# Performance work log

Hardware: AMD Instinct MI355X
Metric: run time of the kernel (lower is better)

## Reference

```python
import jax, jax.numpy as jnp
import numpy as np

N_NODES = 50000
N_EDGES = 600000
D = 128
R = 8
EPS = 1e-5


def layer_norm(x, g, b):
    mu = jnp.mean(x, axis=-1, keepdims=True)
    var = jnp.mean(jnp.square(x - mu), axis=-1, keepdims=True)
    return (x - mu) * jax.lax.rsqrt(var + EPS) * g + b


def rgcn(x, src, dst, edge_attr, W, root, bias, num_nodes):
    # x: [N, d], W: [R, d, f], edge_attr: [E, R] soft relation weights
    E = src.shape[0]
    f = W.shape[-1]
    msg = jnp.zeros((E, f), dtype=x.dtype)
    for r in range(W.shape[0]):  # small fixed relation count
        hr = x @ W[r]                       # [N, f]
        msg = msg + hr[src] * edge_attr[:, r][:, None]  # gather + weight
    agg = jax.ops.segment_sum(msg, dst, num_segments=num_nodes)  # scatter-add
    return agg + x @ root + bias


def setup_inputs() -> dict:
    key = jax.random.key(0)
    ks = jax.random.split(key, 12)
    s = 1.0 / np.sqrt(D)
    return {
        "x": jax.random.normal(ks[0], (N_NODES, D), dtype=jnp.float32),
        "edge_index": jax.random.randint(ks[1], (2, N_EDGES), 0, N_NODES, dtype=jnp.int64),
        "edge_attr": jax.random.uniform(ks[2], (N_EDGES, R), dtype=jnp.float32),
        "ln1_g": jnp.ones((D,), jnp.float32),
        "ln1_b": jnp.zeros((D,), jnp.float32),
        "W1": jax.random.normal(ks[3], (R, D, D), jnp.float32) * s,
        "root1": jax.random.normal(ks[4], (D, D), jnp.float32) * s,
        "b1": jnp.zeros((D,), jnp.float32),
        "ln2_g": jnp.ones((D,), jnp.float32),
        "ln2_b": jnp.zeros((D,), jnp.float32),
        "W2": jax.random.normal(ks[5], (R, D, D), jnp.float32) * s,
        "root2": jax.random.normal(ks[6], (D, D), jnp.float32) * s,
        "b2": jnp.zeros((D,), jnp.float32),
    }


def reference(x, edge_index, edge_attr, ln1_g, ln1_b, W1, root1, b1,
              ln2_g, ln2_b, W2, root2, b2):
    src, dst = edge_index[0], edge_index[1]
    identity = x
    out = jax.nn.gelu(layer_norm(x, ln1_g, ln1_b), approximate=False)
    out = rgcn(out, src, dst, edge_attr, W1, root1, b1, x.shape[0])
    out = jax.nn.gelu(layer_norm(out, ln2_g, ln2_b), approximate=False)
    out = rgcn(out, src, dst, edge_attr, W2, root2, b2, x.shape[0])
    return out + identity
```

## Files before the change

### kernel.cpp

```cpp
#include <hip/hip_runtime.h>
#include <hip/hip_bf16.h>

typedef __attribute__((ext_vector_type(8))) short short8;
typedef __attribute__((ext_vector_type(4))) float f32x4;

#define LDA 1152

__device__ __forceinline__ float bf2f(unsigned short u) {
    union { unsigned int i; float f; } v; v.i = ((unsigned int)u) << 16; return v.f;
}
__device__ __forceinline__ unsigned short f2bf(float f) {
    __hip_bfloat16 h = __float2bfloat16(f);
    union { __hip_bfloat16 h; unsigned short u; } v; v.h = h; return v.u;
}
__device__ __forceinline__ float gelu_exact(float t) {
    return 0.5f * t * (1.0f + erff(t * 0.70710678118654752f));
}

__global__ void prep_all(const float* __restrict__ W1, const float* __restrict__ root1,
                         unsigned short* __restrict__ Bf1,
                         const float* __restrict__ W2, const float* __restrict__ root2,
                         unsigned short* __restrict__ Bf2,
                         int* __restrict__ cnt, int cntB,
                         const float* __restrict__ x, const float* __restrict__ g,
                         const float* __restrict__ bvec, unsigned short* __restrict__ A,
                         int N) {
    int b = blockIdx.x;
    if (b < 1152) {
        int i = b * 256 + threadIdx.x;
        const float* W = W1; const float* root = root1; unsigned short* Bfrag = Bf1;
        if (i >= 1152 * 128) { i -= 1152 * 128; W = W2; root = root2; Bfrag = Bf2; }
        int kp = i >> 7, n = i & 127;
        float v;
        if (kp < 1024) {
            int d = kp >> 3, r = kp & 7;
            v = W[((size_t)r * 128 + d) * 128 + n];
        } else {
            v = root[(size_t)(kp - 1024) * 128 + n];
        }
        int kb = kp >> 5;
        int lane = (((kp >> 3) & 3) << 4) | (n & 15);
        int j = kp & 7;
        int t = n >> 4;
        Bfrag[(((size_t)(kb * 8 + t) * 64 + lane) << 3) + j] = f2bf(v);
        return;
    }
    if (b < 1152 + cntB) {
        int zi = (b - 1152) * 256 + threadIdx.x;
        cnt[zi] = 0;
        return;
    }
    int row = (((b - 1152 - cntB) * 256) + threadIdx.x) >> 6;
    if (row >= N) return;
    int lane = threadIdx.x & 63;
    float2 v = *(const float2*)(x + (size_t)row * 128 + lane * 2);
    float s = v.x + v.y;
    #pragma unroll
    for (int o = 32; o; o >>= 1) s += __shfl_xor(s, o);
    float mu = s * (1.0f / 128.0f);
    float d0 = v.x - mu, d1 = v.y - mu;
    float q = d0 * d0 + d1 * d1;
    #pragma unroll
    for (int o = 32; o; o >>= 1) q += __shfl_xor(q, o);
    float rs = rsqrtf(q * (1.0f / 128.0f) + 1e-5f);
    float2 gg = *(const float2*)(g + lane * 2);
    float2 bb = *(const float2*)(bvec + lane * 2);
    ushort2 o2;
    o2.x = f2bf(gelu_exact(d0 * rs * gg.x + bb.x));
    o2.y = f2bf(gelu_exact(d1 * rs * gg.y + bb.y));
    *(ushort2*)(A + (size_t)row * LDA + 1024 + lane * 2) = o2;
}

__global__ void hist_dst(const int* __restrict__ ei, int* __restrict__ cnt, int E) {
    int e = blockIdx.x * 256 + threadIdx.x;
    if (e >= E) return;
    atomicAdd(&cnt[ei[E + e]], 1);
}

__global__ void scan1(const int* __restrict__ cnt, int* __restrict__ part,
                      int* __restrict__ bsum, int N) {
    int i = blockIdx.x * 256 + threadIdx.x;
    int v = (i < N) ? cnt[i] : 0;
    int lane = threadIdx.x & 63, wid = threadIdx.x >> 6;
    int s = v;
    #pragma unroll
    for (int off = 1; off < 64; off <<= 1) {
        int t = __shfl_up(s, off);
        if (lane >= off) s += t;
    }
    __shared__ int wsum[4];
    if (lane == 63) wsum[wid] = s;
    __syncthreads();
    int add = 0;
    for (int w = 0; w < wid; ++w) add += wsum[w];
    s += add;
    part[i] = s - v;
    if (threadIdx.x == 255) bsum[blockIdx.x] = s;
}

__global__ void scan3(const int* __restrict__ part, const int* __restrict__ bsum,
                      int* __restrict__ rowptr, int* __restrict__ woff, int N) {
    __shared__ int base_sh;
    int b = blockIdx.x;
    if (threadIdx.x < 64) {
        int acc = 0;
        for (int j = threadIdx.x; j < b; j += 64) acc += bsum[j];
        #pragma unroll
        for (int o = 32; o; o >>= 1) acc += __shfl_xor(acc, o);
        if (threadIdx.x == 0) base_sh = acc;
    }
    __syncthreads();
    int i = b * 256 + threadIdx.x;
    if (i >= N) return;
    int v = part[i] + base_sh;
    rowptr[i] = v;
    woff[i] = v;
}

__global__ void scatter_edges(const int* __restrict__ ei, const float4* __restrict__ attr,
                              int* __restrict__ woff, int* __restrict__ esrc,
                              short8* __restrict__ eattr, int E) {
    int e = blockIdx.x * 256 + threadIdx.x;
    if (e >= E) return;
    int src = ei[e], dst = ei[E + e];
    float4 a0 = attr[2 * e], a1 = attr[2 * e + 1];
    short8 pk;
    pk[0] = (short)f2bf(a0.x); pk[1] = (short)f2bf(a0.y);
    pk[2] = (short)f2bf(a0.z); pk[3] = (short)f2bf(a0.w);
    pk[4] = (short)f2bf(a1.x); pk[5] = (short)f2bf(a1.y);
    pk[6] = (short)f2bf(a1.z); pk[7] = (short)f2bf(a1.w);
    int p = atomicAdd(&woff[dst], 1);
    esrc[p] = src;
    eattr[p] = pk;
}

__global__ __launch_bounds__(256) void edge_z(const int* __restrict__ rowptr,
                                              const int* __restrict__ esrc,
                                              const short8* __restrict__ eattr,
                                              unsigned short* __restrict__ A, int N, int E) {
    int row = (blockIdx.x << 2) + (threadIdx.x >> 6);
    if (row >= N) return;
    int lane = threadIdx.x & 63;
    int e0 = rowptr[row];
    int e1 = (row + 1 < N) ? rowptr[row + 1] : E;
    float a0[8] = {0,0,0,0,0,0,0,0};
    float a1[8] = {0,0,0,0,0,0,0,0};
    const unsigned short* yl = A + 1024 + lane * 2;

    #define EDGE_FMA(hv, ea) do {                                      \
        float y0 = bf2f((unsigned short)((hv) & 0xffffu));             \
        float y1 = bf2f((unsigned short)((hv) >> 16));                 \
        _Pragma("unroll")                                              \
        for (int r = 0; r < 8; ++r) {                                  \
            float wv = bf2f((unsigned short)(ea)[r]);                  \
            a0[r] += wv * y0; a1[r] += wv * y1;                        \
        }                                                              \
    } while (0)

    int e = e0;
    for (; e + 4 <= e1; e += 4) {
        unsigned int h[4];
        short8 ea[4];
        #pragma unroll
        for (int u = 0; u < 4; ++u) {
            h[u] = *(const unsigned int*)(yl + (size_t)esrc[e + u] * LDA);
            ea[u] = eattr[e + u];
        }
        #pragma unroll
        for (int u = 0; u < 4; ++u) EDGE_FMA(h[u], ea[u]);
    }
    for (; e < e1; ++e) {
        unsigned int h = *(const unsigned int*)(yl + (size_t)esrc[e] * LDA);
        short8 ea = eattr[e];
        EDGE_FMA(h, ea);
    }
    #undef EDGE_FMA

    short8 p0, p1;
    #pragma unroll
    for (int r = 0; r < 8; ++r) { p0[r] = (short)f2bf(a0[r]); p1[r] = (short)f2bf(a1[r]); }
    unsigned short* zr = A + (size_t)row * LDA + lane * 16;
    *(short8*)zr = p0;
    *(short8*)(zr + 8) = p1;
}

template <int MODE>
__global__ __launch_bounds__(256) void gemm_fused(
        unsigned short* __restrict__ A, const unsigned short* __restrict__ Bfrag,
        const float* __restrict__ bias, const float* __restrict__ lng,
        const float* __restrict__ lnb, const float* __restrict__ xres,
        float* __restrict__ outp, int N) {
    __shared__ short8 Bs[2][1024];

    int w = threadIdx.x >> 6;
    int lane = threadIdx.x & 63;
    int l15 = lane & 15, lhi = lane >> 4;
    int m0 = blockIdx.x * 64 + w * 16;

    const unsigned short* ap = A + (size_t)(m0 + l15) * LDA + lhi * 8;
    const short8* bfb = (const short8*)Bfrag;

    #define STAGE(buf, c)                                                          \
        do {                                                                       \
            const short8* gsrc = bfb + (size_t)(c) * 1024 + w * 64;                \
            _Pragma("unroll")                                                      \
            for (int i = 0; i < 4; ++i)                                            \
                __builtin_amdgcn_global_load_lds(&gsrc[i * 256 + lane],            \
                                                 &Bs[buf][w * 64 + i * 256], 16, 0, 0); \
        } while (0)

    #define BARRIER_CNT2()                                                          \
        do {                                                                        \
            asm volatile("s_waitcnt vmcnt(2)" ::: "memory");                        \
            __builtin_amdgcn_sched_barrier(0);                                      \
            __builtin_amdgcn_s_barrier();                                           \
            __builtin_amdgcn_sched_barrier(0);                                      \
        } while (0)

    short8 af[2], afn[2];
    STAGE(0, 0);
    __builtin_amdgcn_sched_barrier(0);
    #pragma unroll
    for (int k = 0; k < 2; ++k) af[k] = *(const short8*)(ap + k * 32);
    __builtin_amdgcn_sched_barrier(0);
    BARRIER_CNT2();

    f32x4 acc[8] = {};
    for (int c = 0; c < 18; ++c) {
        int cur = c & 1;
        if (c < 17) {
            STAGE(cur ^ 1, c + 1);
            __builtin_amdgcn_sched_barrier(0);
            #pragma unroll
            for (int k = 0; k < 2; ++k)
                afn[k] = *(const short8*)(ap + ((c + 1) * 2 + k) * 32);
            __builtin_amdgcn_sched_barrier(0);
        }
        __builtin_amdgcn_s_setprio(1);
        #pragma unroll
        for (int k = 0; k < 2; ++k) {
            #pragma unroll
            for (int t = 0; t < 8; ++t) {
                short8 b = Bs[cur][k * 512 + t * 64 + lane];
                acc[t] = __builtin_amdgcn_mfma_f32_16x16x32_bf16(af[k], b, acc[t], 0, 0, 0);
            }
        }
        __builtin_amdgcn_s_setprio(0);
        if (c < 17) {
            BARRIER_CNT2();
            af[0] = afn[0]; af[1] = afn[1];
        }
    }
    #undef STAGE
    #undef BARRIER_CNT2

    float bcol[8];
    #pragma unroll
    for (int t = 0; t < 8; ++t) bcol[t] = bias[t * 16 + l15];

    if (MODE == 0) {
        float gcol[8], lbcol[8];
        #pragma unroll
        for (int t = 0; t < 8; ++t) { gcol[t] = lng[t * 16 + l15]; lbcol[t] = lnb[t * 16 + l15]; }
        #pragma unroll
        for (int reg = 0; reg < 4; ++reg) {
            int row = m0 + lhi * 4 + reg;
            float tv[8];
            float s = 0.f;
            #pragma unroll
            for (int t = 0; t < 8; ++t) { tv[t] = acc[t][reg] + bcol[t]; s += tv[t]; }
            #pragma unroll
            for (int msk = 1; msk < 16; msk <<= 1) s += __shfl_xor(s, msk);
            float mu = s * (1.0f / 128.0f);
            float q = 0.f;
            #pragma unroll
            for (int t = 0; t < 8; ++t) { float d = tv[t] - mu; q += d * d; }
            #pragma unroll
            for (int msk = 1; msk < 16; msk <<= 1) q += __shfl_xor(q, msk);
            float rs = rsqrtf(q * (1.0f / 128.0f) + 1e-5f);
            if (row < N) {
                #pragma unroll
                for (int t = 0; t < 8; ++t) {
                    float u = gelu_exact((tv[t] - mu) * rs * gcol[t] + lbcol[t]);
                    A[(size_t)row * LDA + 1024 + t * 16 + l15] = f2bf(u);
                }
            }
        }
    } else {
        #pragma unroll
        for (int reg = 0; reg < 4; ++reg) {
            int row = m0 + lhi * 4 + reg;
            if (row < N) {
                #pragma unroll
                for (int t = 0; t < 8; ++t) {
                    size_t idx = (size_t)row * 128 + t * 16 + l15;
                    outp[idx] = acc[t][reg] + bcol[t] + xres[idx];
                }
            }
        }
    }
}

extern "C" void kernel_launch(void* const* d_in, const int* in_sizes, int n_in,
                              void* d_out, int out_size, void* d_ws, size_t ws_size,
                              hipStream_t stream) {
    const float* x     = (const float*)d_in[0];
    const int*   ei    = (const int*)d_in[1];
    const float* attr  = (const float*)d_in[2];
    const float* ln1g  = (const float*)d_in[3];
    const float* ln1b  = (const float*)d_in[4];
    const float* W1    = (const float*)d_in[5];
    const float* root1 = (const float*)d_in[6];
    const float* b1    = (const float*)d_in[7];
    const float* ln2g  = (const float*)d_in[8];
    const float* ln2b  = (const float*)d_in[9];
    const float* W2    = (const float*)d_in[10];
    const float* root2 = (const float*)d_in[11];
    const float* b2    = (const float*)d_in[12];

    const int N = in_sizes[0] / 128;
    const int E = in_sizes[1] / 2;

    char* ws = (char*)d_ws;
    unsigned short* A     = (unsigned short*)(ws);
    unsigned short* Bf1   = (unsigned short*)(ws + 115400000);
    unsigned short* Bf2   = (unsigned short*)(ws + 115700000);
    int*            cnt   = (int*)(ws + 116000000);
    int*            part  = (int*)(ws + 116210000);
    int*            bsum  = (int*)(ws + 116420000);
    int*            rowptr= (int*)(ws + 116430000);
    int*            woff  = (int*)(ws + 116640000);
    int*            esrc  = (int*)(ws + 116850000);
    short8*         eattr = (short8*)(ws + 119250000);

    const int scanBlocks  = (N + 255) / 256;
    const int edgeBlocksE = (E + 255) / 256;
    const int rowsBlocks  = (N * 64 + 255) / 256;
    const int nodeBlocks  = (N + 3) / 4;
    const int gemmBlocks  = (N + 63) / 64;
    const int prepBlocks  = 1152 + scanBlocks + rowsBlocks;

    prep_all<<<prepBlocks, 256, 0, stream>>>(W1, root1, Bf1, W2, root2, Bf2,
                                             cnt, scanBlocks,
                                             x, ln1g, ln1b, A, N);

    hist_dst<<<edgeBlocksE, 256, 0, stream>>>(ei, cnt, E);
    scan1<<<scanBlocks, 256, 0, stream>>>(cnt, part, bsum, N);
    scan3<<<scanBlocks, 256, 0, stream>>>(part, bsum, rowptr, woff, N);
    scatter_edges<<<edgeBlocksE, 256, 0, stream>>>(ei, (const float4*)attr, woff, esrc, eattr, E);

    edge_z<<<nodeBlocks, 256, 0, stream>>>(rowptr, esrc, eattr, A, N, E);
    gemm_fused<0><<<gemmBlocks, 256, 0, stream>>>(A, Bf1, b1, ln2g, ln2b, nullptr, nullptr, N);

    edge_z<<<nodeBlocks, 256, 0, stream>>>(rowptr, esrc, eattr, A, N, E);
    gemm_fused<1><<<gemmBlocks, 256, 0, stream>>>(A, Bf2, b2, nullptr, nullptr, x, (float*)d_out, N);
}
```

Before: 242.2 us.

## Pad atomic counters and split edge scatter into index scatter plus attribute permute

Histogram and write-offset counters are padded to 16 ints per node so atomics from different nodes no longer share cache lines. The scatter kernel now writes only (src, edge id) pairs, and a separate permute kernel gathers and converts the edge attributes in CSR order, so the attribute stores become coalesced. In exchange there is an extra launch, a 16x larger counter array to zero, strided counter reads in the scan, and edge_z now reads 8-byte pairs instead of 4-byte source ids.

```diff
diff --git a/kernel.cpp b/kernel.cpp
--- a/kernel.cpp
+++ b/kernel.cpp
@@ -5,6 +5,7 @@
 typedef __attribute__((ext_vector_type(4))) float f32x4;
 
 #define LDA 1152
+#define CPAD 16
 
 __device__ __forceinline__ float bf2f(unsigned short u) {
     union { unsigned int i; float f; } v; v.i = ((unsigned int)u) << 16; return v.f;
@@ -21,7 +22,7 @@
                          unsigned short* __restrict__ Bf1,
                          const float* __restrict__ W2, const float* __restrict__ root2,
                          unsigned short* __restrict__ Bf2,
-                         int* __restrict__ cnt, int cntB,
+                         int* __restrict__ cnt, int cntN,
                          const float* __restrict__ x, const float* __restrict__ g,
                          const float* __restrict__ bvec, unsigned short* __restrict__ A,
                          int N) {
@@ -45,9 +46,10 @@
         Bfrag[(((size_t)(kb * 8 + t) * 64 + lane) << 3) + j] = f2bf(v);
         return;
     }
+    int cntB = (cntN + 255) >> 8;
     if (b < 1152 + cntB) {
         int zi = (b - 1152) * 256 + threadIdx.x;
-        cnt[zi] = 0;
+        if (zi < cntN) cnt[zi] = 0;
         return;
     }
     int row = (((b - 1152 - cntB) * 256) + threadIdx.x) >> 6;
@@ -74,13 +76,13 @@
 __global__ void hist_dst(const int* __restrict__ ei, int* __restrict__ cnt, int E) {
     int e = blockIdx.x * 256 + threadIdx.x;
     if (e >= E) return;
-    atomicAdd(&cnt[ei[E + e]], 1);
+    atomicAdd(&cnt[ei[E + e] * CPAD], 1);
 }
 
 __global__ void scan1(const int* __restrict__ cnt, int* __restrict__ part,
                       int* __restrict__ bsum, int N) {
     int i = blockIdx.x * 256 + threadIdx.x;
-    int v = (i < N) ? cnt[i] : 0;
+    int v = (i < N) ? cnt[i * CPAD] : 0;
     int lane = threadIdx.x & 63, wid = threadIdx.x >> 6;
     int s = v;
     #pragma unroll
@@ -114,28 +116,35 @@
     if (i >= N) return;
     int v = part[i] + base_sh;
     rowptr[i] = v;
-    woff[i] = v;
-}
-
-__global__ void scatter_edges(const int* __restrict__ ei, const float4* __restrict__ attr,
-                              int* __restrict__ woff, int* __restrict__ esrc,
-                              short8* __restrict__ eattr, int E) {
+    woff[i * CPAD] = v;
+}
+
+__global__ void scatter_edges(const int* __restrict__ ei, int* __restrict__ woff,
+                              int2* __restrict__ esp, int E) {
     int e = blockIdx.x * 256 + threadIdx.x;
     if (e >= E) return;
     int src = ei[e], dst = ei[E + e];
+    int p = atomicAdd(&woff[dst * CPAD], 1);
+    int2 v; v.x = src; v.y = e;
+    esp[p] = v;
+}
+
+__global__ void permute_attr(const int2* __restrict__ esp, const float4* __restrict__ attr,
+                             short8* __restrict__ eattr, int E) {
+    int p = blockIdx.x * 256 + threadIdx.x;
+    if (p >= E) return;
+    int e = esp[p].y;
     float4 a0 = attr[2 * e], a1 = attr[2 * e + 1];
     short8 pk;
     pk[0] = (short)f2bf(a0.x); pk[1] = (short)f2bf(a0.y);
     pk[2] = (short)f2bf(a0.z); pk[3] = (short)f2bf(a0.w);
     pk[4] = (short)f2bf(a1.x); pk[5] = (short)f2bf(a1.y);
     pk[6] = (short)f2bf(a1.z); pk[7] = (short)f2bf(a1.w);
-    int p = atomicAdd(&woff[dst], 1);
-    esrc[p] = src;
     eattr[p] = pk;
 }
 
 __global__ __launch_bounds__(256) void edge_z(const int* __restrict__ rowptr,
-                                              const int* __restrict__ esrc,
+                                              const int2* __restrict__ esp,
                                               const short8* __restrict__ eattr,
                                               unsigned short* __restrict__ A, int N, int E) {
     int row = (blockIdx.x << 2) + (threadIdx.x >> 6);
@@ -163,14 +172,14 @@
         short8 ea[4];
         #pragma unroll
         for (int u = 0; u < 4; ++u) {
-            h[u] = *(const unsigned int*)(yl + (size_t)esrc[e + u] * LDA);
+            h[u] = *(const unsigned int*)(yl + (size_t)esp[e + u].x * LDA);
             ea[u] = eattr[e + u];
         }
         #pragma unroll
         for (int u = 0; u < 4; ++u) EDGE_FMA(h[u], ea[u]);
     }
     for (; e < e1; ++e) {
-        unsigned int h = *(const unsigned int*)(yl + (size_t)esrc[e] * LDA);
+        unsigned int h = *(const unsigned int*)(yl + (size_t)esp[e].x * LDA);
         short8 ea = eattr[e];
         EDGE_FMA(h, ea);
     }
@@ -326,32 +335,35 @@
     unsigned short* Bf1   = (unsigned short*)(ws + 115400000);
     unsigned short* Bf2   = (unsigned short*)(ws + 115700000);
     int*            cnt   = (int*)(ws + 116000000);
-    int*            part  = (int*)(ws + 116210000);
-    int*            bsum  = (int*)(ws + 116420000);
-    int*            rowptr= (int*)(ws + 116430000);
-    int*            woff  = (int*)(ws + 116640000);
-    int*            esrc  = (int*)(ws + 116850000);
-    short8*         eattr = (short8*)(ws + 119250000);
+    int*            part  = (int*)(ws + 119220000);
+    int*            bsum  = (int*)(ws + 119430000);
+    int*            rowptr= (int*)(ws + 119440000);
+    int*            woff  = (int*)(ws + 119650000);
+    int2*           esp   = (int2*)(ws + 122870000);
+    short8*         eattr = (short8*)(ws + 127680000);
 
     const int scanBlocks  = (N + 255) / 256;
     const int edgeBlocksE = (E + 255) / 256;
     const int rowsBlocks  = (N * 64 + 255) / 256;
     const int nodeBlocks  = (N + 3) / 4;
     const int gemmBlocks  = (N + 63) / 64;
-    const int prepBlocks  = 1152 + scanBlocks + rowsBlocks;
+    const int cntN        = scanBlocks * 256 * CPAD;
+    const int cntB        = (cntN + 255) / 256;
+    const int prepBlocks  = 1152 + cntB + rowsBlocks;
 
     prep_all<<<prepBlocks, 256, 0, stream>>>(W1, root1, Bf1, W2, root2, Bf2,
-                                             cnt, scanBlocks,
+                                             cnt, cntN,
                                              x, ln1g, ln1b, A, N);
 
     hist_dst<<<edgeBlocksE, 256, 0, stream>>>(ei, cnt, E);
     scan1<<<scanBlocks, 256, 0, stream>>>(cnt, part, bsum, N);
     scan3<<<scanBlocks, 256, 0, stream>>>(part, bsum, rowptr, woff, N);
-    scatter_edges<<<edgeBlocksE, 256, 0, stream>>>(ei, (const float4*)attr, woff, esrc, eattr, E);
-
-    edge_z<<<nodeBlocks, 256, 0, stream>>>(rowptr, esrc, eattr, A, N, E);
+    scatter_edges<<<edgeBlocksE, 256, 0, stream>>>(ei, woff, esp, E);
+    permute_attr<<<edgeBlocksE, 256, 0, stream>>>(esp, (const float4*)attr, eattr, E);
+
+    edge_z<<<nodeBlocks, 256, 0, stream>>>(rowptr, esp, eattr, A, N, E);
     gemm_fused<0><<<gemmBlocks, 256, 0, stream>>>(A, Bf1, b1, ln2g, ln2b, nullptr, nullptr, N);
 
-    edge_z<<<nodeBlocks, 256, 0, stream>>>(rowptr, esrc, eattr, A, N, E);
+    edge_z<<<nodeBlocks, 256, 0, stream>>>(rowptr, esp, eattr, A, N, E);
     gemm_fused<1><<<gemmBlocks, 256, 0, stream>>>(A, Bf2, b2, nullptr, nullptr, x, (float*)d_out, N);
 }
```

Measured after the change: 253.4 us. +4.6%, slower.
